# Optimization experiments

Measured on AMD Instinct MI355X. Metric: run time of the kernel, lower is better.

## Reference

```python
import jax, jax.numpy as jnp
import numpy as np
from jax import lax

B, S, H, T = 64, 512, 1024, 21


def setup_inputs() -> dict:
    key = jax.random.key(0)
    k1, k2, k3, k4, k5, k6, k7 = jax.random.split(key, 7)
    hidden_states = jax.random.normal(k1, (B, S, H), dtype=jnp.float32)
    attention_mask = jnp.ones((B, S), dtype=jnp.int32)
    labels = jax.random.randint(k2, (B, S), 0, T).astype(jnp.int64)
    W = jax.random.normal(k3, (T, H), dtype=jnp.float32) * 0.02
    b = jnp.zeros((T,), dtype=jnp.float32)
    # torchcrf init: uniform(-0.1, 0.1)
    transitions = jax.random.uniform(k4, (T, T), minval=-0.1, maxval=0.1, dtype=jnp.float32)
    start_transitions = jax.random.uniform(k5, (T,), minval=-0.1, maxval=0.1, dtype=jnp.float32)
    end_transitions = jax.random.uniform(k6, (T,), minval=-0.1, maxval=0.1, dtype=jnp.float32)
    return {
        "hidden_states": hidden_states,
        "attention_mask": attention_mask,
        "labels": labels,
        "W": W,
        "b": b,
        "transitions": transitions,
        "start_transitions": start_transitions,
        "end_transitions": end_transitions,
    }


def _crf_log_likelihood(emissions, labels, mask, trans, start, end):
    # emissions [B,S,T], labels [B,S] int, mask [B,S] bool. reduction='sum'.
    Bn, Sn, Tn = emissions.shape
    maskf = mask.astype(emissions.dtype)
    emit_scores = jnp.take_along_axis(emissions, labels[:, :, None], axis=2)[:, :, 0]  # [B,S]
    trans_scores = trans[labels[:, :-1], labels[:, 1:]]  # [B,S-1]
    numerator = start[labels[:, 0]] + emit_scores[:, 0]
    numerator = numerator + jnp.sum((trans_scores + emit_scores[:, 1:]) * maskf[:, 1:], axis=1)
    seq_ends = jnp.sum(mask.astype(jnp.int32), axis=1) - 1  # [B]
    last_tags = labels[jnp.arange(Bn), seq_ends]
    numerator = numerator + end[last_tags]
    # partition via forward algorithm (scan over time)
    alpha0 = start[None, :] + emissions[:, 0]  # [B,T]
    def step(alpha, inp):
        emit_t, mask_t = inp  # [B,T], [B]
        nxt = jax.nn.logsumexp(alpha[:, :, None] + trans[None, :, :] + emit_t[:, None, :], axis=1)
        return jnp.where(mask_t[:, None], nxt, alpha), None
    alpha, _ = lax.scan(step, alpha0, (emissions[:, 1:].transpose(1, 0, 2), mask[:, 1:].T))
    log_Z = jax.nn.logsumexp(alpha + end[None, :], axis=1)  # [B]
    return jnp.sum(numerator - log_Z)


def _viterbi_decode(emissions, mask, trans, start, end):
    Bn, Sn, Tn = emissions.shape
    score0 = start[None, :] + emissions[:, 0]  # [B,T]
    identity_bp = jnp.broadcast_to(jnp.arange(Tn)[None, :], (Bn, Tn))
    def fwd(score, inp):
        emit_t, mask_t = inp
        broad = score[:, :, None] + trans[None, :, :]  # [B, prev, cur]
        best_prev = jnp.argmax(broad, axis=1)  # [B,T]
        nxt = jnp.max(broad, axis=1) + emit_t
        new_score = jnp.where(mask_t[:, None], nxt, score)
        bp = jnp.where(mask_t[:, None], best_prev, identity_bp)
        return new_score, bp
    final_score, bps = lax.scan(fwd, score0, (emissions[:, 1:].transpose(1, 0, 2), mask[:, 1:].T))
    last_tag = jnp.argmax(final_score + end[None, :], axis=1)  # [B] tag at pos S-1
    def back(tag, bp_t):
        prev = jnp.take_along_axis(bp_t, tag[:, None], axis=1)[:, 0]
        return prev, tag
    tag0, tags_rest = lax.scan(back, last_tag, bps, reverse=True)  # tags_rest[t] = tag at pos t+1
    tags = jnp.concatenate([tag0[None, :], tags_rest], axis=0).T  # [B,S]
    return jnp.where(mask, tags, 0).astype(jnp.int64)


def reference(hidden_states, attention_mask, labels, W, b, transitions, start_transitions, end_transitions):
    mask = attention_mask.astype(bool)
    # dropout is identity in eval mode
    emissions = jnp.einsum("bsh,th->bst", hidden_states, W) + b  # [B,S,T]
    log_prob = _crf_log_likelihood(emissions, labels, mask, transitions, start_transitions, end_transitions)
    loss = -log_prob
    pred = _viterbi_decode(emissions, mask, transitions, start_transitions, end_transitions)
    return loss, pred
```

## Files before the change

### kernel.cpp

```cpp
#include <hip/hip_runtime.h>
#include <math.h>
#include <stdint.h>

#define BB 64
#define SS 512
#define HH 1024
#define TT 21

template <int CTRL>
__device__ __forceinline__ float dpp_add(float v) {
  int t = __builtin_amdgcn_update_dpp(0, __float_as_int(v), CTRL, 0xF, 0xF, true);
  return v + __int_as_float(t);
}
__device__ __forceinline__ float wave_sum(float v) {
  v = dpp_add<0x121>(v);
  v = dpp_add<0x122>(v);
  v = dpp_add<0x124>(v);
  v = dpp_add<0x128>(v);
  v += __shfl_xor(v, 16);
  v += __shfl_xor(v, 32);
  return v;
}

#define DOT4(A, H, WV)    \
  A = fmaf(H.x, WV.x, A); \
  A = fmaf(H.y, WV.y, A); \
  A = fmaf(H.z, WV.z, A); \
  A = fmaf(H.w, WV.w, A)

__global__ __launch_bounds__(512, 2) void k_emis(const float* __restrict__ hs,
                                                 const float* __restrict__ W,
                                                 const float* __restrict__ bias,
                                                 float* __restrict__ emis) {
  __shared__ float sW[TT * HH];
  __shared__ float sB[TT];
  {
    const float4* Wv = (const float4*)W;
    float4* sWv = (float4*)sW;
    for (int i = threadIdx.x; i < TT * HH / 4; i += 512) sWv[i] = Wv[i];
    if (threadIdx.x < TT) sB[threadIdx.x] = bias[threadIdx.x];
  }
  __syncthreads();
  const int lane = threadIdx.x & 63;
  const int wid = threadIdx.x >> 6;
  const int gw = blockIdx.x * 8 + wid;
  for (int g = 0; g < 4; ++g) {
    const int row0 = gw * 8 + g * 2;
    const float4* hp0 = (const float4*)(hs + (size_t)row0 * HH);
    const float4* hp1 = (const float4*)(hs + (size_t)(row0 + 1) * HH);
    float4 h0[4], h1[4];
#pragma unroll
    for (int c = 0; c < 4; ++c) {
      h0[c] = hp0[c * 64 + lane];
      h1[c] = hp1[c * 64 + lane];
    }
    float* ep0 = emis + (size_t)row0 * TT;
    float* ep1 = ep0 + TT;
#pragma unroll 1
    for (int tg = 0; tg < TT; tg += 3) {
      float a00 = 0.f, a01 = 0.f, a02 = 0.f;
      float a10 = 0.f, a11 = 0.f, a12 = 0.f;
#pragma unroll
      for (int c = 0; c < 4; ++c) {
        float4 w0 = ((const float4*)(sW + (tg + 0) * HH))[c * 64 + lane];
        float4 w1 = ((const float4*)(sW + (tg + 1) * HH))[c * 64 + lane];
        float4 w2 = ((const float4*)(sW + (tg + 2) * HH))[c * 64 + lane];
        DOT4(a00, h0[c], w0);
        DOT4(a01, h0[c], w1);
        DOT4(a02, h0[c], w2);
        DOT4(a10, h1[c], w0);
        DOT4(a11, h1[c], w1);
        DOT4(a12, h1[c], w2);
      }
      a00 = wave_sum(a00);
      a01 = wave_sum(a01);
      a02 = wave_sum(a02);
      a10 = wave_sum(a10);
      a11 = wave_sum(a11);
      a12 = wave_sum(a12);
      if (lane == 0) {
        ep0[tg] = a00 + sB[tg];
        ep0[tg + 1] = a01 + sB[tg + 1];
        ep0[tg + 2] = a02 + sB[tg + 2];
      }
      if (lane == 1) {
        ep1[tg] = a10 + sB[tg];
        ep1[tg + 1] = a11 + sB[tg + 1];
        ep1[tg + 2] = a12 + sB[tg + 2];
      }
    }
  }
}

__global__ __launch_bounds__(64, 1) void k_scan(const float* __restrict__ emis,
                                                const int* __restrict__ mask,
                                                const float* __restrict__ trans,
                                                const float* __restrict__ sv,
                                                const float* __restrict__ ev,
                                                float* __restrict__ logZ,
                                                float* __restrict__ pred) {
  __shared__ float sE[2 * SS * TT];
  __shared__ int sM[2 * SS];
  __shared__ unsigned char bp[2][SS][32];
  __shared__ unsigned char sTag[2][SS];
  __shared__ float sV[2][24];
  const int lane = threadIdx.x;
  const int g = lane >> 5;
  const int j = lane & 31;
  const bool act = (j < TT);
  const int jj = act ? j : 0;
  const int b0 = (blockIdx.x & 31) * 2;
  const int b = b0 + g;

  if (lane < 48) ((float*)sV)[lane] = 0.f;

  {
    const float4* src = (const float4*)(emis + (size_t)b0 * SS * TT);
    float4* dst = (float4*)sE;
    for (int i = lane; i < 2 * SS * TT / 4; i += 64) dst[i] = src[i];
    const int* msrc = mask + b0 * SS;
    for (int i = lane; i < 2 * SS; i += 64) sM[i] = msrc[i];
  }
  __syncthreads();
  const float* myE = sE + g * SS * TT;
  const int* myM = sM + g * SS;

  if (blockIdx.x < 32) {
    float E[TT];
#pragma unroll
    for (int i = 0; i < TT; ++i) E[i] = __expf(trans[i * TT + jj]);
    float v = act ? __expf(sv[jj] + myE[jj]) : 0.f;
    float C = 0.f;
    float ge_nx = __expf(myE[TT + jj]);
    int mk_nx = myM[1];
    for (int t = 1; t < SS; ++t) {
      const float ge = ge_nx;
      const int mk = mk_nx;
      const int tn = (t + 1 < SS) ? (t + 1) : (SS - 1);
      ge_nx = __expf(myE[tn * TT + jj]);
      mk_nx = myM[tn];
      if (act) sV[g][j] = v;
      __syncthreads();
      const float4* vb = (const float4*)sV[g];
      float4 V0 = vb[0], V1 = vb[1], V2 = vb[2], V3 = vb[3], V4 = vb[4], V5 = vb[5];
      float scale = 1.0f;
      if ((t & 7) == 0) {
        float m = fmaxf(fmaxf(fmaxf(V0.x, V0.y), fmaxf(V0.z, V0.w)),
                        fmaxf(fmaxf(V1.x, V1.y), fmaxf(V1.z, V1.w)));
        m = fmaxf(m, fmaxf(fmaxf(V2.x, V2.y), fmaxf(V2.z, V2.w)));
        m = fmaxf(m, fmaxf(fmaxf(V3.x, V3.y), fmaxf(V3.z, V3.w)));
        m = fmaxf(m, fmaxf(fmaxf(V4.x, V4.y), fmaxf(V4.z, V4.w)));
        m = fmaxf(m, V5.x);
        int ex = (int)((__float_as_uint(m) >> 23) & 255u) - 127;
        scale = __uint_as_float((unsigned)(127 - ex) << 23);
        C += (float)ex * 0.6931471805599453f;
        v *= scale;
      }
      float q0 = V0.x * E[0], q1 = V0.y * E[1], q2 = V0.z * E[2];
      q0 = fmaf(V0.w, E[3], q0);  q1 = fmaf(V1.x, E[4], q1);  q2 = fmaf(V1.y, E[5], q2);
      q0 = fmaf(V1.z, E[6], q0);  q1 = fmaf(V1.w, E[7], q1);  q2 = fmaf(V2.x, E[8], q2);
      q0 = fmaf(V2.y, E[9], q0);  q1 = fmaf(V2.z, E[10], q1); q2 = fmaf(V2.w, E[11], q2);
      q0 = fmaf(V3.x, E[12], q0); q1 = fmaf(V3.y, E[13], q1); q2 = fmaf(V3.z, E[14], q2);
      q0 = fmaf(V3.w, E[15], q0); q1 = fmaf(V4.x, E[16], q1); q2 = fmaf(V4.y, E[17], q2);
      q0 = fmaf(V4.z, E[18], q0); q1 = fmaf(V4.w, E[19], q1); q2 = fmaf(V5.x, E[20], q2);
      float vn = ((q0 + q1 + q2) * scale) * ge;
      v = (act && mk) ? vn : v;
    }
    float wv = act ? v * __expf(ev[jj]) : 0.f;
#pragma unroll
    for (int d = 16; d >= 1; d >>= 1) wv += __shfl_xor(wv, d);
    if (j == 0) logZ[b] = C + __logf(wv);
  } else {
    float Tc[TT];
#pragma unroll
    for (int i = 0; i < TT; ++i) Tc[i] = trans[i * TT + jj];
    float sc = act ? (sv[jj] + myE[jj]) : -3.0e38f;
    float e_nx = myE[TT + jj];
    int mk_nx = myM[1];
    for (int t = 1; t < SS; ++t) {
      const float e = e_nx;
      const int mk = mk_nx;
      const int tn = (t + 1 < SS) ? (t + 1) : (SS - 1);
      e_nx = myE[tn * TT + jj];
      mk_nx = myM[tn];
      if (act) sV[g][j] = sc;
      __syncthreads();
      const float4* vb = (const float4*)sV[g];
      float4 V0 = vb[0], V1 = vb[1], V2 = vb[2], V3 = vb[3], V4 = vb[4], V5 = vb[5];
      float b0v, b1v, b2v;
      int i0, i1, i2;
#define ARGSTEP(BV, BI, VAL, IDX)          \
  {                                        \
    float x_ = (VAL) + Tc[IDX];            \
    if (x_ > BV) { BV = x_; BI = (IDX); }  \
  }
      b0v = V0.x + Tc[0]; i0 = 0;
      b1v = V0.y + Tc[1]; i1 = 1;
      b2v = V0.z + Tc[2]; i2 = 2;
      ARGSTEP(b0v, i0, V0.w, 3);  ARGSTEP(b1v, i1, V1.x, 4);  ARGSTEP(b2v, i2, V1.y, 5);
      ARGSTEP(b0v, i0, V1.z, 6);  ARGSTEP(b1v, i1, V1.w, 7);  ARGSTEP(b2v, i2, V2.x, 8);
      ARGSTEP(b0v, i0, V2.y, 9);  ARGSTEP(b1v, i1, V2.z, 10); ARGSTEP(b2v, i2, V2.w, 11);
      ARGSTEP(b0v, i0, V3.x, 12); ARGSTEP(b1v, i1, V3.y, 13); ARGSTEP(b2v, i2, V3.z, 14);
      ARGSTEP(b0v, i0, V3.w, 15); ARGSTEP(b1v, i1, V4.x, 16); ARGSTEP(b2v, i2, V4.y, 17);
      ARGSTEP(b0v, i0, V4.z, 18); ARGSTEP(b1v, i1, V4.w, 19); ARGSTEP(b2v, i2, V5.x, 20);
#undef ARGSTEP
      float best = b0v;
      int bi = i0;
      if (b1v > best || (b1v == best && i1 < bi)) { best = b1v; bi = i1; }
      if (b2v > best || (b2v == best && i2 < bi)) { best = b2v; bi = i2; }
      float ns = best + e;
      sc = (act && mk) ? ns : sc;
      bp[g][t][j] = (unsigned char)(mk ? bi : j);
    }
    float fsv = act ? (sc + ev[jj]) : -3.0e38f;
    int idx = j;
#pragma unroll
    for (int d = 16; d >= 1; d >>= 1) {
      float ov = __shfl_xor(fsv, d);
      int oi = __shfl_xor(idx, d);
      bool take = (ov > fsv) || (ov == fsv && oi < idx);
      fsv = take ? ov : fsv;
      idx = take ? oi : idx;
    }
    __syncthreads();
    if (j == 0) {
      int tag = idx;
      sTag[g][SS - 1] = (unsigned char)tag;
      for (int t = SS - 1; t >= 1; --t) {
        tag = bp[g][t][tag];
        sTag[g][t - 1] = (unsigned char)tag;
      }
    }
    __syncthreads();
    for (int i = lane; i < 2 * SS; i += 64) {
      pred[(size_t)b0 * SS + i] = (float)(sM[i] ? (int)sTag[i >> 9][i & (SS - 1)] : 0);
    }
  }
}

__global__ __launch_bounds__(64, 1) void k_loss(const float* __restrict__ emis,
                                                const int* __restrict__ mask,
                                                const int* __restrict__ labels,
                                                const float* __restrict__ trans,
                                                const float* __restrict__ sv,
                                                const float* __restrict__ ev,
                                                const float* __restrict__ logZ,
                                                float* __restrict__ outv) {
  const int b = blockIdx.x;
  const int lane = threadIdx.x;
  float p = 0.f;
  int cnt = 0;
  for (int t = lane; t < SS; t += 64) {
    cnt += mask[b * SS + t] ? 1 : 0;
    if (t >= 1) {
      const int lp = labels[b * SS + t - 1];
      const int lc = labels[b * SS + t];
      const float mk = (float)mask[b * SS + t];
      p += mk * (trans[lp * TT + lc] + emis[((size_t)b * SS + t) * TT + lc]);
    }
  }
  p = wave_sum(p);
#pragma unroll
  for (int d = 32; d >= 1; d >>= 1) cnt += __shfl_xor(cnt, d);
  if (lane == 0) {
    const int l0 = labels[b * SS];
    float numer = p + sv[l0] + emis[(size_t)b * SS * TT + l0];
    numer += ev[labels[b * SS + cnt - 1]];
    atomicAdd(outv, logZ[b] - numer);
  }
}

extern "C" void kernel_launch(void* const* d_in, const int* in_sizes, int n_in,
                              void* d_out, int out_size, void* d_ws, size_t ws_size,
                              hipStream_t stream) {
  const float* hs = (const float*)d_in[0];
  const int* msk = (const int*)d_in[1];
  const int* lab = (const int*)d_in[2];
  const float* W = (const float*)d_in[3];
  const float* bias = (const float*)d_in[4];
  const float* trans = (const float*)d_in[5];
  const float* sv = (const float*)d_in[6];
  const float* ev = (const float*)d_in[7];
  float* out = (float*)d_out;

  float* emis = (float*)d_ws;
  float* logZ = emis + (size_t)BB * SS * TT;

  hipMemsetAsync(d_out, 0, 4, stream);
  k_emis<<<512, 512, 0, stream>>>(hs, W, bias, emis);
  k_scan<<<64, 64, 0, stream>>>(emis, msk, trans, sv, ev, logZ, out + 1);
  k_loss<<<64, 64, 0, stream>>>(emis, msk, lab, trans, sv, ev, logZ, out);
}
```

Measured before the change: 466.5 us.

## Restructure emission GEMV to per-thread register accumulators with W read from global

The emission projection no longer stages the 84 KB weight matrix into shared memory per block. Instead, 8 threads cooperate on each row, each holding 21 register accumulators over a strided slice of H and reading W directly through the cache. Partial sums are reduced through a small shared buffer, replacing the wave-wide DPP reductions. This removes the per-block W copy and the shuffle reductions, at the cost of higher register pressure and non-coalesced hidden-state loads (8 lanes per row, 32 rows per block).

New measurement: 731.3 us. 56.8% more time.

```diff
diff --git a/kernel.cpp b/kernel.cpp
--- a/kernel.cpp
+++ b/kernel.cpp
@@ -28,67 +28,46 @@
   A = fmaf(H.z, WV.z, A); \
   A = fmaf(H.w, WV.w, A)
 
-__global__ __launch_bounds__(512, 2) void k_emis(const float* __restrict__ hs,
+#define RPB 32
+__global__ __launch_bounds__(256, 4) void k_emis(const float* __restrict__ hs,
                                                  const float* __restrict__ W,
                                                  const float* __restrict__ bias,
                                                  float* __restrict__ emis) {
-  __shared__ float sW[TT * HH];
-  __shared__ float sB[TT];
-  {
-    const float4* Wv = (const float4*)W;
-    float4* sWv = (float4*)sW;
-    for (int i = threadIdx.x; i < TT * HH / 4; i += 512) sWv[i] = Wv[i];
-    if (threadIdx.x < TT) sB[threadIdx.x] = bias[threadIdx.x];
-  }
+  __shared__ float part[256 * TT];
+  const int tid = threadIdx.x;
+  const int q = tid & 7;
+  const int r = tid >> 3;
+  const size_t row = (size_t)blockIdx.x * RPB + r;
+  const float4* hp = (const float4*)(hs + row * HH);
+
+  float acc[TT];
+#pragma unroll
+  for (int t = 0; t < TT; ++t) acc[t] = 0.f;
+
+  float4 h = hp[q];
+#pragma unroll 2
+  for (int i = 0; i < 32; ++i) {
+    const float4 hc = h;
+    if (i < 31) h = hp[(i + 1) * 8 + q];
+    const float* wb = W + (size_t)(i * 8 + q) * 4;
+#pragma unroll
+    for (int t = 0; t < TT; ++t) {
+      const float4 w = *(const float4*)(wb + t * HH);
+      DOT4(acc[t], hc, w);
+    }
+  }
+
+#pragma unroll
+  for (int t = 0; t < TT; ++t) part[tid * TT + t] = acc[t];
   __syncthreads();
-  const int lane = threadIdx.x & 63;
-  const int wid = threadIdx.x >> 6;
-  const int gw = blockIdx.x * 8 + wid;
-  for (int g = 0; g < 4; ++g) {
-    const int row0 = gw * 8 + g * 2;
-    const float4* hp0 = (const float4*)(hs + (size_t)row0 * HH);
-    const float4* hp1 = (const float4*)(hs + (size_t)(row0 + 1) * HH);
-    float4 h0[4], h1[4];
-#pragma unroll
-    for (int c = 0; c < 4; ++c) {
-      h0[c] = hp0[c * 64 + lane];
-      h1[c] = hp1[c * 64 + lane];
-    }
-    float* ep0 = emis + (size_t)row0 * TT;
-    float* ep1 = ep0 + TT;
-#pragma unroll 1
-    for (int tg = 0; tg < TT; tg += 3) {
-      float a00 = 0.f, a01 = 0.f, a02 = 0.f;
-      float a10 = 0.f, a11 = 0.f, a12 = 0.f;
-#pragma unroll
-      for (int c = 0; c < 4; ++c) {
-        float4 w0 = ((const float4*)(sW + (tg + 0) * HH))[c * 64 + lane];
-        float4 w1 = ((const float4*)(sW + (tg + 1) * HH))[c * 64 + lane];
-        float4 w2 = ((const float4*)(sW + (tg + 2) * HH))[c * 64 + lane];
-        DOT4(a00, h0[c], w0);
-        DOT4(a01, h0[c], w1);
-        DOT4(a02, h0[c], w2);
-        DOT4(a10, h1[c], w0);
-        DOT4(a11, h1[c], w1);
-        DOT4(a12, h1[c], w2);
-      }
-      a00 = wave_sum(a00);
-      a01 = wave_sum(a01);
-      a02 = wave_sum(a02);
-      a10 = wave_sum(a10);
-      a11 = wave_sum(a11);
-      a12 = wave_sum(a12);
-      if (lane == 0) {
-        ep0[tg] = a00 + sB[tg];
-        ep0[tg + 1] = a01 + sB[tg + 1];
-        ep0[tg + 2] = a02 + sB[tg + 2];
-      }
-      if (lane == 1) {
-        ep1[tg] = a10 + sB[tg];
-        ep1[tg + 1] = a11 + sB[tg + 1];
-        ep1[tg + 2] = a12 + sB[tg + 2];
-      }
-    }
+
+  for (int o = tid; o < RPB * TT; o += 256) {
+    const int rr = o / TT;
+    const int t = o - rr * TT;
+    const float* pp = part + (size_t)(rr * 8) * TT + t;
+    float s = ((pp[0] + pp[TT]) + (pp[2 * TT] + pp[3 * TT])) +
+              ((pp[4 * TT] + pp[5 * TT]) + (pp[6 * TT] + pp[7 * TT]));
+    emis[(size_t)blockIdx.x * RPB * TT + o] = s + bias[t];
   }
 }
 
@@ -287,7 +266,7 @@
   float* logZ = emis + (size_t)BB * SS * TT;
 
   hipMemsetAsync(d_out, 0, 4, stream);
-  k_emis<<<512, 512, 0, stream>>>(hs, W, bias, emis);
+  k_emis<<<1024, 256, 0, stream>>>(hs, W, bias, emis);
   k_scan<<<64, 64, 0, stream>>>(emis, msk, trans, sv, ev, logZ, out + 1);
   k_loss<<<64, 64, 0, stream>>>(emis, msk, lab, trans, sv, ev, logZ, out);
 }
```
